# Kernel tuning notes

Hardware: AMD Instinct MI355X
Metric: run time of the kernel (lower is better)

## Reference

```python
import jax, jax.numpy as jnp
import numpy as np


def _bilinear_align_corners(img, H_out, W_out):
    # img: [B, C, h, w] -> [B, C, H_out, W_out], matching F.interpolate(mode='bilinear', align_corners=True)
    b, c, h, w = img.shape
    ys = jnp.linspace(0.0, h - 1.0, H_out)
    xs = jnp.linspace(0.0, w - 1.0, W_out)
    y0 = jnp.floor(ys).astype(jnp.int32)
    x0 = jnp.floor(xs).astype(jnp.int32)
    y1 = jnp.minimum(y0 + 1, h - 1)
    x1 = jnp.minimum(x0 + 1, w - 1)
    wy = (ys - y0)[:, None]          # [H_out, 1]
    wx = (xs - x0)[None, :]          # [1, W_out]

    def gather(yi, xi):
        return img[:, :, yi, :][:, :, :, xi]  # [B, C, H_out, W_out]

    top = gather(y0, x0) * (1.0 - wx) + gather(y0, x1) * wx
    bot = gather(y1, x0) * (1.0 - wx) + gather(y1, x1) * wx
    return top * (1.0 - wy) + bot * wy


def _conv1x1(x, W, b):
    # x: [B, C, H, W_], W: [O, C], b: [O]
    return jnp.einsum('bchw,oc->bohw', x, W) + b[None, :, None, None]


def setup_inputs() -> dict:
    key = jax.random.key(0)
    ks = jax.random.split(key, 9)
    B, C, H, W = 4, 256, 64, 64
    C8 = C // 8
    s_qk = 1.0 / np.sqrt(C)
    return {
        'x': jax.random.normal(ks[0], (B, C, H, W), dtype=jnp.float32),
        'guiding_map0': jax.random.normal(ks[1], (B, 1, 32, 32), dtype=jnp.float32),
        'Wq': jax.random.normal(ks[2], (C8, C), dtype=jnp.float32) * s_qk,
        'bq': jax.random.normal(ks[3], (C8,), dtype=jnp.float32) * 0.01,
        'Wk': jax.random.normal(ks[4], (C8, C), dtype=jnp.float32) * s_qk,
        'bk': jax.random.normal(ks[5], (C8,), dtype=jnp.float32) * 0.01,
        'Wv': jax.random.normal(ks[6], (C, C), dtype=jnp.float32) * s_qk,
        'bv': jax.random.normal(ks[7], (C,), dtype=jnp.float32) * 0.01,
        'gamma': jax.random.normal(ks[8], (1,), dtype=jnp.float32) * 0.1,
    }


def reference(x, guiding_map0, Wq, bq, Wk, bk, Wv, bv, gamma):
    B, C, H, W = x.shape
    N = H * W
    # upsample guiding map to x's spatial size, then sigmoid gate
    gm = jax.nn.sigmoid(_bilinear_align_corners(guiding_map0, H, W))  # [B,1,H,W]
    gate = 1.0 + gm

    q = (_conv1x1(x, Wq, bq) * gate).reshape(B, -1, N)  # [B, C//8, N]
    k = (_conv1x1(x, Wk, bk) * gate).reshape(B, -1, N)  # [B, C//8, N]
    v = (_conv1x1(x, Wv, bv) * gate).reshape(B, C, N)   # [B, C, N]

    # energy[b, n, m] = q[b, :, n] . k[b, :, m]
    energy = jnp.einsum('bcn,bcm->bnm', q, k)           # [B, N, N]
    attention = jax.nn.softmax(energy, axis=-1)
    # out[b, c, n] = sum_m v[b, c, m] * attention[b, n, m]
    out = jnp.einsum('bcm,bnm->bcn', v, attention).reshape(B, C, H, W)
    return gamma[0] * out + x
```

## Files before the change

kernel.cpp:

```cpp
#include <hip/hip_runtime.h>
#include <hip/hip_bf16.h>
#include <cstdint>

typedef __attribute__((ext_vector_type(4)))  float f32x4;
typedef __attribute__((ext_vector_type(16))) float f32x16;
typedef __attribute__((ext_vector_type(8)))  short s16x8;

#define LOG2E 1.4426950408889634f
#define RESC_THR 8.0f

#define B_   4
#define C_   256
#define N_   4096
#define NT_  256
#define MB_  128
#define QG_  128

#define WS_WFRAG 0u
#define WS_BIAS  163840u
#define WS_Q     262144u
#define WS_K     1310720u
#define WS_V     2359296u
#define WS_PART  11534336u
#define WS_ML    45088768u
#define WS_NEED  45613056ull

__device__ __forceinline__ short bf16s(float f) {
  return (short)__bfloat16_as_ushort(__float2bfloat16(f));
}
__device__ __forceinline__ float bf2f(short h) {
  union { unsigned u; float f; } v; v.u = ((unsigned)(unsigned short)h) << 16;
  return v.f;
}
__device__ __forceinline__ void gl_lds16(const void* g, void* l) {
  __builtin_amdgcn_global_load_lds(
      (const __attribute__((address_space(1))) unsigned int*)g,
      (__attribute__((address_space(3))) unsigned int*)l, 16, 0, 0);
}

__global__ void wprep_kernel(const float* __restrict__ Wq, const float* __restrict__ Wk,
                             const float* __restrict__ Wv, const float* __restrict__ bq,
                             const float* __restrict__ bk, const float* __restrict__ bv,
                             short* __restrict__ wfrag, float* __restrict__ bias) {
  int d0 = blockIdx.x * 256 + threadIdx.x;
  int d = d0;
  int j  = d & 7;  d >>= 3;
  int c  = d & 15; d >>= 4;
  int g  = d & 3;  d >>= 2;
  int ks = d & 7;  d >>= 3;
  int t  = d;
  int o  = t * 16 + c;
  int ch = ks * 32 + g * 8 + j;
  float w = (o < 32) ? Wq[o * 256 + ch] : (o < 64) ? Wk[(o - 32) * 256 + ch]
                                                   : Wv[(o - 64) * 256 + ch];
  wfrag[d0] = bf16s(w);
  if (d0 < 320) bias[d0] = (d0 < 32) ? bq[d0] : (d0 < 64) ? bk[d0 - 32] : bv[d0 - 64];
}

__global__ __launch_bounds__(256) void proj_kernel(
    const float* __restrict__ x, const short* __restrict__ wfrag,
    const float* __restrict__ bias, const float* __restrict__ gm,
    short* __restrict__ qs, short* __restrict__ ksz, short* __restrict__ vs) {
  int b = blockIdx.x >> 8, nt = blockIdx.x & 255;
  int lane = threadIdx.x & 63, wave = threadIdx.x >> 6;
  int g = lane >> 4, c = lane & 15;
  int n = nt * 16 + c;

  float gt;
  {
    int y = n >> 6, xp = n & 63;
    float fy = (float)(y * 31) / 63.0f;
    float fx = (float)(xp * 31) / 63.0f;
    int y0 = (int)fy, x0 = (int)fx;
    float wy = fy - (float)y0, wx = fx - (float)x0;
    int y1 = min(y0 + 1, 31), x1 = min(x0 + 1, 31);
    const float* p = gm + b * 1024;
    float v00 = p[y0 * 32 + x0], v01 = p[y0 * 32 + x1];
    float v10 = p[y1 * 32 + x0], v11 = p[y1 * 32 + x1];
    float top = v00 * (1.f - wx) + v01 * wx;
    float bot = v10 * (1.f - wx) + v11 * wx;
    float gv  = top * (1.f - wy) + bot * wy;
    gt = 1.0f + 1.0f / (1.0f + expf(-gv));
  }

  const float* xb = x + b * (C_ * N_) + n;
  s16x8 xf[8];
  #pragma unroll
  for (int ks = 0; ks < 8; ++ks) {
    int ch0 = ks * 32 + g * 8;
    s16x8 v;
    #pragma unroll
    for (int j = 0; j < 8; ++j) v[j] = bf16s(xb[(ch0 + j) * N_]);
    xf[ks] = v;
  }

  int qt32 = n >> 5, r = n & 31;
  for (int t = wave * 5; t < wave * 5 + 5; ++t) {
    f32x4 acc = {0.f, 0.f, 0.f, 0.f};
    #pragma unroll
    for (int ks = 0; ks < 8; ++ks) {
      s16x8 wf = *(const s16x8*)(wfrag + ((((t * 8 + ks) * 4 + g) * 16 + c) * 8));
      acc = __builtin_amdgcn_mfma_f32_16x16x32_bf16(wf, xf[ks], acc, 0, 0, 0);
    }
    #pragma unroll
    for (int jj = 0; jj < 4; ++jj) {
      int o = t * 16 + g * 4 + jj;
      float val = (acc[jj] + bias[o]) * gt;
      short bv16 = bf16s(val);
      if (o < 64) {
        int ch = o & 31;
        int s  = (ch >> 4) & 1, hi = (ch >> 3) & 1, j = ch & 7;
        short* dst = (o < 32) ? qs : ksz;
        dst[(((b * QG_ + qt32) * 2 + s) * 64 + hi * 32 + r) * 8 + j] = bv16;
      } else {
        int cv = o - 64;
        int ct = cv >> 5, lam = cv & 31;
        int s  = (r >> 4) & 1, r4 = r & 15;
        int k  = (r4 & 3) | (((r4 >> 3) & 1) << 2) | (((r4 >> 2) & 1) << 3);
        int hi = k >> 3, j = k & 7;
        vs[((((size_t)(b * MB_ + qt32) * 8 + ct) * 2 + s) * 64 + hi * 32 + lam) * 8 + j] = bv16;
      }
    }
  }
}

__global__ __launch_bounds__(512, 2) void attn_split_kernel(
    const short* __restrict__ qs, const short* __restrict__ ksz,
    const short* __restrict__ vs, short* __restrict__ part,
    float* __restrict__ mlbuf) {
  __shared__ __align__(16) short k_lds[2][1024];
  __shared__ __align__(16) short v_lds[2][8192];

  int bid = blockIdx.x;
  int b  = (bid & 7) >> 1;
  int u  = ((bid >> 3) << 1) | (bid & 1);
  int qb = u >> 2, s = u & 3;
  int tid = threadIdx.x, lane = tid & 63, wave = tid >> 6;
  int lq = lane & 31, hi = lane >> 5;
  int qt = qb * 8 + wave;

  const short* qbp = qs + (size_t)(((b * QG_ + qt) * 2) * 64 + lane) * 8;
  s16x8 qf0 = *(const s16x8*)(qbp);
  s16x8 qf1 = *(const s16x8*)(qbp + 512);

  f32x16 acc[8];
  #pragma unroll
  for (int ct = 0; ct < 8; ++ct)
    #pragma unroll
    for (int e = 0; e < 16; ++e) acc[ct][e] = 0.f;
  float m = -3.0e38f, lsum = 0.f;

  const char* kbase = (const char*)(ksz + (size_t)b * (MB_ * 1024));
  const char* vbase = (const char*)(vs + (size_t)b * ((size_t)MB_ * 8192));

  #define STAGE(mb, nb)                                                          \
    {                                                                            \
      const char* vsrc = vbase + (size_t)(mb) * 16384;                           \
      gl_lds16(vsrc + (wave * 2 + 0) * 1024 + lane * 16,                         \
               &v_lds[nb][(wave * 2 + 0) * 512]);                                \
      gl_lds16(vsrc + (wave * 2 + 1) * 1024 + lane * 16,                         \
               &v_lds[nb][(wave * 2 + 1) * 512]);                                \
      if (wave < 2) {                                                            \
        const char* ksrc = kbase + (size_t)(mb) * 2048;                          \
        gl_lds16(ksrc + wave * 1024 + lane * 16, &k_lds[nb][wave * 512]);        \
      }                                                                          \
    }

  STAGE(s * 32, 0);
  __syncthreads();

  for (int i = 0; i < 32; ++i) {
    int cur = i & 1;
    if (i < 31) STAGE(s * 32 + i + 1, cur ^ 1);

    const short* kb = k_lds[cur];
    s16x8 kf0 = *(const s16x8*)(kb + lane * 8);
    s16x8 kf1 = *(const s16x8*)(kb + 512 + lane * 8);
    f32x16 st;
    #pragma unroll
    for (int e = 0; e < 16; ++e) st[e] = 0.f;
    st = __builtin_amdgcn_mfma_f32_32x32x16_bf16(kf0, qf0, st, 0, 0, 0);
    st = __builtin_amdgcn_mfma_f32_32x32x16_bf16(kf1, qf1, st, 0, 0, 0);

    float pm = st[0];
    #pragma unroll
    for (int e = 1; e < 16; ++e) pm = fmaxf(pm, st[e]);
    pm = fmaxf(pm, __shfl_xor(pm, 32));

    if (!__all(pm <= m + RESC_THR)) {
      float mnew = fmaxf(m, pm);
      float scale = exp2f((m - mnew) * LOG2E);
      lsum *= scale;
      #pragma unroll
      for (int ct = 0; ct < 8; ++ct)
        #pragma unroll
        for (int e = 0; e < 16; ++e) acc[ct][e] *= scale;
      m = mnew;
    }

    float psum = 0.f;
    s16x8 pf0, pf1;
    #pragma unroll
    for (int j = 0; j < 8; ++j) {
      float p = exp2f((st[j] - m) * LOG2E);
      psum += p; pf0[j] = bf16s(p);
    }
    #pragma unroll
    for (int j = 0; j < 8; ++j) {
      float p = exp2f((st[8 + j] - m) * LOG2E);
      psum += p; pf1[j] = bf16s(p);
    }
    psum += __shfl_xor(psum, 32);
    lsum += psum;

    const short* vb = v_lds[cur];
    #pragma unroll
    for (int ct = 0; ct < 8; ++ct) {
      s16x8 vf0 = *(const s16x8*)(vb + (ct * 2 + 0) * 512 + lane * 8);
      s16x8 vf1 = *(const s16x8*)(vb + (ct * 2 + 1) * 512 + lane * 8);
      acc[ct] = __builtin_amdgcn_mfma_f32_32x32x16_bf16(vf0, pf0, acc[ct], 0, 0, 0);
      acc[ct] = __builtin_amdgcn_mfma_f32_32x32x16_bf16(vf1, pf1, acc[ct], 0, 0, 0);
    }
    __syncthreads();
  }

  int pt = (b * 128 + qt) * 4 + s;
  if (lane < 32) {
    mlbuf[pt * 64 + lq]      = m;
    mlbuf[pt * 64 + 32 + lq] = lsum;
  }
  short* pb = part + (size_t)pt * 8192;
  #pragma unroll
  for (int ct = 0; ct < 8; ++ct)
    #pragma unroll
    for (int e = 0; e < 16; ++e) {
      int CH = ct * 32 + (e & 3) + 8 * (e >> 2) + 4 * hi;
      pb[CH * 32 + lq] = bf16s(acc[ct][e]);
    }
  #undef STAGE
}

__global__ __launch_bounds__(256) void combine_kernel(
    const short* __restrict__ part, const float* __restrict__ mlbuf,
    const float* __restrict__ x, const float* __restrict__ gamma,
    float* __restrict__ out) {
  int bid = blockIdx.x;
  int b = bid >> 7, qt = bid & 127;
  int t = threadIdx.x;
  int q = t & 31, cg = t >> 5;
  int base = (b * 128 + qt) * 4;
  float m0 = mlbuf[(base + 0) * 64 + q], m1 = mlbuf[(base + 1) * 64 + q];
  float m2 = mlbuf[(base + 2) * 64 + q], m3 = mlbuf[(base + 3) * 64 + q];
  float M = fmaxf(fmaxf(m0, m1), fmaxf(m2, m3));
  float w0 = exp2f((m0 - M) * LOG2E), w1 = exp2f((m1 - M) * LOG2E);
  float w2 = exp2f((m2 - M) * LOG2E), w3 = exp2f((m3 - M) * LOG2E);
  float L = mlbuf[(base + 0) * 64 + 32 + q] * w0 + mlbuf[(base + 1) * 64 + 32 + q] * w1
          + mlbuf[(base + 2) * 64 + 32 + q] * w2 + mlbuf[(base + 3) * 64 + 32 + q] * w3;
  float rn = gamma[0] / L;
  int n = qt * 32 + q;
  const short* p0 = part + (size_t)(base + 0) * 8192;
  const short* p1 = part + (size_t)(base + 1) * 8192;
  const short* p2 = part + (size_t)(base + 2) * 8192;
  const short* p3 = part + (size_t)(base + 3) * 8192;
  #pragma unroll 4
  for (int cc = 0; cc < 32; ++cc) {
    int ch = cg * 32 + cc;
    int off = ch * 32 + q;
    float o = w0 * bf2f(p0[off]) + w1 * bf2f(p1[off])
            + w2 * bf2f(p2[off]) + w3 * bf2f(p3[off]);
    int idx = (b * C_ + ch) * N_ + n;
    out[idx] = rn * o + x[idx];
  }
}

__global__ __launch_bounds__(256, 2) void attn_reg_kernel(
    const short* __restrict__ qs, const short* __restrict__ ksz,
    const short* __restrict__ vs, const float* __restrict__ x,
    const float* __restrict__ gamma, float* __restrict__ out) {
  __shared__ float comb_m[4][32];
  __shared__ float comb_l[4][32];
  __shared__ float sumbuf[4][16][4][64];

  int bid = blockIdx.x;
  int b  = (bid & 7) >> 1;
  int qg = ((bid >> 3) << 1) | (bid & 1);
  int tid = threadIdx.x, lane = tid & 63, wave = tid >> 6;
  int lq = lane & 31;

  const short* qb = qs + (size_t)(((b * QG_ + qg) * 2) * 64 + lane) * 8;
  s16x8 qf0 = *(const s16x8*)(qb);
  s16x8 qf1 = *(const s16x8*)(qb + 512);

  f32x16 acc[8];
  #pragma unroll
  for (int ct = 0; ct < 8; ++ct)
    #pragma unroll
    for (int e = 0; e < 16; ++e) acc[ct][e] = 0.f;
  float m = -3.0e38f, lsum = 0.f;

  const short* kb0 = ksz + (size_t)b * (MB_ * 1024) + lane * 8;
  const short* vb0 = vs  + (size_t)b * ((size_t)MB_ * 8192) + lane * 8;

  int mb = wave;
  s16x8 kf0 = *(const s16x8*)(kb0 + mb * 1024);
  s16x8 kf1 = *(const s16x8*)(kb0 + mb * 1024 + 512);

  for (int i = 0; i < 32; ++i) {
    const short* vb = vb0 + (size_t)mb * 8192;
    s16x8 vf[16];
    #pragma unroll
    for (int t = 0; t < 16; ++t) vf[t] = *(const s16x8*)(vb + t * 512);

    f32x16 st;
    #pragma unroll
    for (int e = 0; e < 16; ++e) st[e] = 0.f;
    st = __builtin_amdgcn_mfma_f32_32x32x16_bf16(kf0, qf0, st, 0, 0, 0);
    st = __builtin_amdgcn_mfma_f32_32x32x16_bf16(kf1, qf1, st, 0, 0, 0);

    int mbn = (i < 31) ? (mb + 4) : wave;
    s16x8 nk0 = *(const s16x8*)(kb0 + mbn * 1024);
    s16x8 nk1 = *(const s16x8*)(kb0 + mbn * 1024 + 512);

    float pm = st[0];
    #pragma unroll
    for (int e = 1; e < 16; ++e) pm = fmaxf(pm, st[e]);
    pm = fmaxf(pm, __shfl_xor(pm, 32));

    if (!__all(pm <= m + RESC_THR)) {
      float mnew = fmaxf(m, pm);
      float scale = exp2f((m - mnew) * LOG2E);
      lsum *= scale;
      #pragma unroll
      for (int ct = 0; ct < 8; ++ct)
        #pragma unroll
        for (int e = 0; e < 16; ++e) acc[ct][e] *= scale;
      m = mnew;
    }

    float psum = 0.f;
    s16x8 pf0, pf1;
    #pragma unroll
    for (int j = 0; j < 8; ++j) {
      float p = exp2f((st[j] - m) * LOG2E);
      psum += p; pf0[j] = bf16s(p);
    }
    #pragma unroll
    for (int j = 0; j < 8; ++j) {
      float p = exp2f((st[8 + j] - m) * LOG2E);
      psum += p; pf1[j] = bf16s(p);
    }
    psum += __shfl_xor(psum, 32);
    lsum += psum;

    #pragma unroll
    for (int ct = 0; ct < 8; ++ct) {
      acc[ct] = __builtin_amdgcn_mfma_f32_32x32x16_bf16(vf[ct * 2],     pf0, acc[ct], 0, 0, 0);
      acc[ct] = __builtin_amdgcn_mfma_f32_32x32x16_bf16(vf[ct * 2 + 1], pf1, acc[ct], 0, 0, 0);
    }
    kf0 = nk0; kf1 = nk1; mb = mbn;
  }

  if (lane < 32) { comb_m[wave][lq] = m; comb_l[wave][lq] = lsum; }
  __syncthreads();
  float M = fmaxf(fmaxf(comb_m[0][lq], comb_m[1][lq]),
                  fmaxf(comb_m[2][lq], comb_m[3][lq]));
  float L = 0.f;
  #pragma unroll
  for (int w2 = 0; w2 < 4; ++w2)
    L += comb_l[w2][lq] * exp2f((comb_m[w2][lq] - M) * LOG2E);
  float myscale = exp2f((m - M) * LOG2E);
  float rn = gamma[0] / L;
  int n = qg * 32 + lq;
  int hi = lane >> 5;

  for (int phase = 0; phase < 2; ++phase) {
    #pragma unroll
    for (int t = 0; t < 4; ++t)
      #pragma unroll
      for (int e = 0; e < 16; ++e)
        sumbuf[t][e][wave][lane] = acc[phase * 4 + t][e] * myscale;
    __syncthreads();
    int ct = phase * 4 + wave;
    #pragma unroll
    for (int e = 0; e < 16; ++e) {
      float ssum = sumbuf[wave][e][0][lane] + sumbuf[wave][e][1][lane]
                 + sumbuf[wave][e][2][lane] + sumbuf[wave][e][3][lane];
      int ch = ct * 32 + (e & 3) + 8 * (e >> 2) + 4 * hi;
      int idx = (b * C_ + ch) * N_ + n;
      out[idx] = rn * ssum + x[idx];
    }
    __syncthreads();
  }
}

extern "C" void kernel_launch(void* const* d_in, const int* in_sizes, int n_in,
                              void* d_out, int out_size, void* d_ws, size_t ws_size,
                              hipStream_t stream) {
  const float* x     = (const float*)d_in[0];
  const float* gm    = (const float*)d_in[1];
  const float* Wq    = (const float*)d_in[2];
  const float* bq    = (const float*)d_in[3];
  const float* Wk    = (const float*)d_in[4];
  const float* bk    = (const float*)d_in[5];
  const float* Wv    = (const float*)d_in[6];
  const float* bv    = (const float*)d_in[7];
  const float* gamma = (const float*)d_in[8];

  char*  ws    = (char*)d_ws;
  short* wfrag = (short*)(ws + WS_WFRAG);
  float* bias  = (float*)(ws + WS_BIAS);
  short* qs    = (short*)(ws + WS_Q);
  short* ksz   = (short*)(ws + WS_K);
  short* vs    = (short*)(ws + WS_V);
  float* out   = (float*)d_out;

  wprep_kernel<<<dim3(320), dim3(256), 0, stream>>>(Wq, Wk, Wv, bq, bk, bv, wfrag, bias);
  proj_kernel<<<dim3(1024), dim3(256), 0, stream>>>(x, wfrag, bias, gm, qs, ksz, vs);

  if (ws_size >= WS_NEED) {
    short* part  = (short*)(ws + WS_PART);
    float* mlbuf = (float*)(ws + WS_ML);
    attn_split_kernel<<<dim3(256), dim3(512), 0, stream>>>(qs, ksz, vs, part, mlbuf);
    combine_kernel<<<dim3(512), dim3(256), 0, stream>>>(part, mlbuf, x, gamma, out);
  } else {
    attn_reg_kernel<<<dim3(512), dim3(256), 0, stream>>>(qs, ksz, vs, x, gamma, out);
  }
}
```

Before: 94.87 us.

## Triple-buffer attention K/V staging and software-pipeline QK^T with PV

Attention split kernel moves from double to triple-buffered LDS staging of K/V tiles. The loop is software-pipelined so the next tile's QK^T MFMA issues alongside the current tile's PV accumulation. Full __syncthreads are replaced with raw s_barrier plus explicit vmcnt waits, and s_setprio raises priority around the MFMA block. This aims to hide global-to-LDS latency and softmax ALU work behind matrix ops, at the cost of more LDS (which may limit the two-blocks-per-CU occupancy) and fragile hand-counted vmcnt waits. Redundant reloads of the last tile at the loop tail add a little extra traffic.

```diff
diff --git a/kernel.cpp b/kernel.cpp
--- a/kernel.cpp
+++ b/kernel.cpp
@@ -128,8 +128,8 @@
     const short* __restrict__ qs, const short* __restrict__ ksz,
     const short* __restrict__ vs, short* __restrict__ part,
     float* __restrict__ mlbuf) {
-  __shared__ __align__(16) short k_lds[2][1024];
-  __shared__ __align__(16) short v_lds[2][8192];
+  __shared__ __align__(16) short k_lds[3][1024];
+  __shared__ __align__(16) short v_lds[3][8192];
 
   int bid = blockIdx.x;
   int b  = (bid & 7) >> 1;
@@ -142,6 +142,7 @@
   const short* qbp = qs + (size_t)(((b * QG_ + qt) * 2) * 64 + lane) * 8;
   s16x8 qf0 = *(const s16x8*)(qbp);
   s16x8 qf1 = *(const s16x8*)(qbp + 512);
+  asm volatile("s_waitcnt vmcnt(0)" ::: "memory");
 
   f32x16 acc[8];
   #pragma unroll
@@ -165,63 +166,93 @@
         gl_lds16(ksrc + wave * 1024 + lane * 16, &k_lds[nb][wave * 512]);        \
       }                                                                          \
     }
-
-  STAGE(s * 32, 0);
-  __syncthreads();
-
-  for (int i = 0; i < 32; ++i) {
-    int cur = i & 1;
-    if (i < 31) STAGE(s * 32 + i + 1, cur ^ 1);
-
-    const short* kb = k_lds[cur];
-    s16x8 kf0 = *(const s16x8*)(kb + lane * 8);
-    s16x8 kf1 = *(const s16x8*)(kb + 512 + lane * 8);
-    f32x16 st;
-    #pragma unroll
-    for (int e = 0; e < 16; ++e) st[e] = 0.f;
-    st = __builtin_amdgcn_mfma_f32_32x32x16_bf16(kf0, qf0, st, 0, 0, 0);
-    st = __builtin_amdgcn_mfma_f32_32x32x16_bf16(kf1, qf1, st, 0, 0, 0);
-
-    float pm = st[0];
-    #pragma unroll
-    for (int e = 1; e < 16; ++e) pm = fmaxf(pm, st[e]);
-    pm = fmaxf(pm, __shfl_xor(pm, 32));
-
-    if (!__all(pm <= m + RESC_THR)) {
-      float mnew = fmaxf(m, pm);
-      float scale = exp2f((m - mnew) * LOG2E);
-      lsum *= scale;
-      #pragma unroll
-      for (int ct = 0; ct < 8; ++ct)
-        #pragma unroll
-        for (int e = 0; e < 16; ++e) acc[ct][e] *= scale;
-      m = mnew;
-    }
-
-    float psum = 0.f;
-    s16x8 pf0, pf1;
-    #pragma unroll
-    for (int j = 0; j < 8; ++j) {
-      float p = exp2f((st[j] - m) * LOG2E);
-      psum += p; pf0[j] = bf16s(p);
-    }
-    #pragma unroll
-    for (int j = 0; j < 8; ++j) {
-      float p = exp2f((st[8 + j] - m) * LOG2E);
-      psum += p; pf1[j] = bf16s(p);
-    }
-    psum += __shfl_xor(psum, 32);
-    lsum += psum;
-
-    const short* vb = v_lds[cur];
-    #pragma unroll
-    for (int ct = 0; ct < 8; ++ct) {
-      s16x8 vf0 = *(const s16x8*)(vb + (ct * 2 + 0) * 512 + lane * 8);
-      s16x8 vf1 = *(const s16x8*)(vb + (ct * 2 + 1) * 512 + lane * 8);
-      acc[ct] = __builtin_amdgcn_mfma_f32_32x32x16_bf16(vf0, pf0, acc[ct], 0, 0, 0);
-      acc[ct] = __builtin_amdgcn_mfma_f32_32x32x16_bf16(vf1, pf1, acc[ct], 0, 0, 0);
-    }
-    __syncthreads();
+  #define WAIT_PREV()                                                            \
+    {                                                                            \
+      if (wave < 2) asm volatile("s_waitcnt vmcnt(3)" ::: "memory");             \
+      else          asm volatile("s_waitcnt vmcnt(2)" ::: "memory");             \
+    }
+
+  s16x8 pf0, pf1;
+  f32x16 st;
+
+  #define QKT(buf)                                                               \
+    {                                                                            \
+      const short* kb = k_lds[buf];                                              \
+      s16x8 kf0 = *(const s16x8*)(kb + lane * 8);                                \
+      s16x8 kf1 = *(const s16x8*)(kb + 512 + lane * 8);                          \
+      _Pragma("unroll")                                                          \
+      for (int e = 0; e < 16; ++e) st[e] = 0.f;                                  \
+      st = __builtin_amdgcn_mfma_f32_32x32x16_bf16(kf0, qf0, st, 0, 0, 0);       \
+      st = __builtin_amdgcn_mfma_f32_32x32x16_bf16(kf1, qf1, st, 0, 0, 0);       \
+    }
+
+  #define SOFTMAX()                                                              \
+    {                                                                            \
+      float a0 = fmaxf(st[0], st[1]),  a1 = fmaxf(st[2], st[3]);                 \
+      float a2 = fmaxf(st[4], st[5]),  a3 = fmaxf(st[6], st[7]);                 \
+      float a4 = fmaxf(st[8], st[9]),  a5 = fmaxf(st[10], st[11]);               \
+      float a6 = fmaxf(st[12], st[13]), a7 = fmaxf(st[14], st[15]);              \
+      float b0 = fmaxf(a0, a1), b1 = fmaxf(a2, a3);                              \
+      float b2 = fmaxf(a4, a5), b3 = fmaxf(a6, a7);                              \
+      float pm = fmaxf(fmaxf(b0, b1), fmaxf(b2, b3));                            \
+      pm = fmaxf(pm, __shfl_xor(pm, 32));                                        \
+      if (!__all(pm <= m + RESC_THR)) {                                          \
+        float mnew = fmaxf(m, pm);                                               \
+        float scale = exp2f((m - mnew) * LOG2E);                                 \
+        lsum *= scale;                                                           \
+        _Pragma("unroll")                                                        \
+        for (int ct = 0; ct < 8; ++ct)                                           \
+          _Pragma("unroll")                                                      \
+          for (int e = 0; e < 16; ++e) acc[ct][e] *= scale;                      \
+        m = mnew;                                                                \
+      }                                                                          \
+      float psum = 0.f;                                                          \
+      _Pragma("unroll")                                                          \
+      for (int j = 0; j < 8; ++j) {                                              \
+        float p = exp2f((st[j] - m) * LOG2E);                                    \
+        psum += p; pf0[j] = bf16s(p);                                            \
+      }                                                                          \
+      _Pragma("unroll")                                                          \
+      for (int j = 0; j < 8; ++j) {                                              \
+        float p = exp2f((st[8 + j] - m) * LOG2E);                                \
+        psum += p; pf1[j] = bf16s(p);                                            \
+      }                                                                          \
+      psum += __shfl_xor(psum, 32);                                              \
+      lsum += psum;                                                              \
+    }
+
+  #define PVACC(buf)                                                             \
+    {                                                                            \
+      const short* vb = v_lds[buf];                                              \
+      _Pragma("unroll")                                                          \
+      for (int ct = 0; ct < 8; ++ct) {                                           \
+        s16x8 vf0 = *(const s16x8*)(vb + (ct * 2 + 0) * 512 + lane * 8);         \
+        s16x8 vf1 = *(const s16x8*)(vb + (ct * 2 + 1) * 512 + lane * 8);         \
+        acc[ct] = __builtin_amdgcn_mfma_f32_32x32x16_bf16(vf0, pf0, acc[ct], 0, 0, 0); \
+        acc[ct] = __builtin_amdgcn_mfma_f32_32x32x16_bf16(vf1, pf1, acc[ct], 0, 0, 0); \
+      }                                                                          \
+    }
+
+  STAGE(s * 32 + 0, 0);
+  STAGE(s * 32 + 1, 1);
+  WAIT_PREV();
+  __builtin_amdgcn_s_barrier();
+  QKT(0);
+  SOFTMAX();
+
+  int bc = 0, bn = 1, bs = 2;
+  for (int j = 0; j < 32; ++j) {
+    __builtin_amdgcn_s_barrier();
+    int jn = j + 2; if (jn > 31) jn = 31;
+    STAGE(s * 32 + jn, bs);
+    WAIT_PREV();
+    __builtin_amdgcn_s_barrier();
+    __builtin_amdgcn_s_setprio(1);
+    if (j < 31) QKT(bn);
+    PVACC(bc);
+    __builtin_amdgcn_s_setprio(0);
+    if (j < 31) SOFTMAX();
+    int t = bc; bc = bn; bn = bs; bs = t;
   }
 
   int pt = (b * 128 + qt) * 4 + s;
@@ -238,6 +269,10 @@
       pb[CH * 32 + lq] = bf16s(acc[ct][e]);
     }
   #undef STAGE
+  #undef WAIT_PREV
+  #undef QKT
+  #undef SOFTMAX
+  #undef PVACC
 }
 
 __global__ __launch_bounds__(256) void combine_kernel(
```

Result: slower. 97.57 us (+2.8%).
